# Optimization experiments

Hardware: AMD Instinct MI355X
Metric: run time of the kernel (lower is better)

The kernel has to match this reference:

```python
import jax, jax.numpy as jnp
import numpy as np

B, L = 64, 2048
N_RESTYPE, N_GROUP, N_ATOM = 21, 8, 14


def _compose(R1, t1, R2, t2):
    # rigid compose: (R1,t1) o (R2,t2) = (R1@R2, R1@t2 + t1)
    R = jnp.einsum('...ij,...jk->...ik', R1, R2)
    t = jnp.einsum('...ij,...j->...i', R1, t2) + t1
    return R, t


def setup_inputs() -> dict:
    key = jax.random.key(0)
    ks = jax.random.split(key, 8)
    return {
        'bb_rots': jax.random.normal(ks[0], (B, L, 3, 3), jnp.float32),
        'bb_trans': jax.random.normal(ks[1], (B, L, 3), jnp.float32),
        'angles': jax.random.normal(ks[2], (B, L, 7, 2), jnp.float32),
        'aatype': jax.random.randint(ks[3], (B, L), 0, N_RESTYPE),
        'default_frames': jax.random.normal(ks[4], (N_RESTYPE, N_GROUP, 4, 4), jnp.float32),
        'group_idx': jax.random.randint(ks[5], (N_RESTYPE, N_ATOM), 0, N_GROUP),
        'atom_mask': jax.random.uniform(ks[6], (N_RESTYPE, N_ATOM), jnp.float32),
        'lit_positions': jax.random.normal(ks[7], (N_RESTYPE, N_ATOM, 3), jnp.float32),
    }


def reference(bb_rots, bb_trans, angles, aatype, default_frames, group_idx, atom_mask, lit_positions):
    # ---- torsion_angles_to_frames ----
    d4 = default_frames[aatype]                      # [B,L,8,4,4]
    dR, dt = d4[..., :3, :3], d4[..., :3, 3]
    # prepend identity backbone torsion (sin=0, cos=1)
    bb = jnp.broadcast_to(jnp.array([0.0, 1.0], angles.dtype), (*angles.shape[:-2], 1, 2))
    ang = jnp.concatenate([bb, angles], axis=-2)     # [B,L,8,2]
    s, c = ang[..., 0], ang[..., 1]
    z, o = jnp.zeros_like(s), jnp.ones_like(s)
    # rotation about x-axis built from (sin, cos)
    rotx = jnp.stack([
        jnp.stack([o, z, z], axis=-1),
        jnp.stack([z, c, -s], axis=-1),
        jnp.stack([z, s, c], axis=-1),
    ], axis=-2)                                      # [B,L,8,3,3]
    fR = jnp.einsum('blgij,blgjk->blgik', dR, rotx)  # default_r.compose(all_rots)
    ft = dt                                          # all_rots has zero translation
    # chain chi2..chi4 onto chi1
    R5, t5 = _compose(fR[:, :, 4], ft[:, :, 4], fR[:, :, 5], ft[:, :, 5])
    R6, t6 = _compose(R5, t5, fR[:, :, 6], ft[:, :, 6])
    R7, t7 = _compose(R6, t6, fR[:, :, 7], ft[:, :, 7])
    Rbb = jnp.concatenate([fR[:, :, :5], R5[:, :, None], R6[:, :, None], R7[:, :, None]], axis=2)
    tbb = jnp.concatenate([ft[:, :, :5], t5[:, :, None], t6[:, :, None], t7[:, :, None]], axis=2)
    # compose with global backbone frame
    Rg = jnp.einsum('blij,blgjk->blgik', bb_rots, Rbb)          # [B,L,8,3,3]
    tg = jnp.einsum('blij,blgj->blgi', bb_rots, tbb) + bb_trans[:, :, None]

    # ---- frames_and_literature_positions_to_atom14_pos ----
    gidx = group_idx[aatype]                                    # [B,L,14]
    Ra = jnp.take_along_axis(Rg, gidx[:, :, :, None, None], axis=2)  # [B,L,14,3,3]
    ta = jnp.take_along_axis(tg, gidx[:, :, :, None], axis=2)        # [B,L,14,3]
    lit = lit_positions[aatype]                                 # [B,L,14,3]
    mask = atom_mask[aatype][..., None]                         # [B,L,14,1]
    pred = jnp.einsum('blaij,blaj->blai', Ra, lit) + ta
    return pred * mask
```

## Files before the change

kernel.cpp:

```cpp
#include <hip/hip_runtime.h>


constexpr int NRES_TOTAL = 64 * 2048;
constexpr int NRT = 21;
constexpr int NG  = 8;
constexpr int NA  = 14;
constexpr int OUT_F = NA * 3;
constexpr int BLK = 256;
constexpr int OUT_F4 = BLK * OUT_F / 4;

__global__ __launch_bounds__(256) void protein_mapper_kernel(
    const float* __restrict__ bb_rots,
    const float* __restrict__ bb_trans,
    const float* __restrict__ angles,
    const int*   __restrict__ aatype,
    const float* __restrict__ default_frames,
    const int*   __restrict__ group_idx,
    const float* __restrict__ atom_mask,
    const float* __restrict__ lit_positions,
    float* __restrict__ out)
{
    __shared__ float s_frames[128 * NRT];
    __shared__ int   s_gidx[NA * NRT];
    __shared__ float s_mask[NA * NRT];
    __shared__ float s_lit[NA * 3 * NRT];
    __shared__ float s_out[BLK * OUT_F];

    for (int n = threadIdx.x; n < NRT * 128; n += BLK) {
        const int aa = n / 128, j = n % 128;
        s_frames[j * NRT + aa] = default_frames[n];
    }
    for (int n = threadIdx.x; n < NRT * NA; n += BLK) {
        const int aa = n / NA, a = n % NA;
        s_gidx[a * NRT + aa] = group_idx[n];
        s_mask[a * NRT + aa] = atom_mask[n];
    }
    for (int n = threadIdx.x; n < NRT * NA * 3; n += BLK) {
        const int aa = n / (NA * 3), k = n % (NA * 3);
        s_lit[k * NRT + aa] = lit_positions[n];
    }
    __syncthreads();

    const int i = blockIdx.x * BLK + threadIdx.x;
    const int aa = aatype[i];

    float sv[NG], cv[NG];
    sv[0] = 0.0f; cv[0] = 1.0f;
    const float2* angp = reinterpret_cast<const float2*>(angles + (size_t)i * 14);
    #pragma unroll
    for (int g = 1; g < NG; ++g) {
        float2 sc = angp[g - 1];
        sv[g] = sc.x;
        cv[g] = sc.y;
    }

    float G[NG][12];
    #pragma unroll
    for (int g = 0; g < NG; ++g) {
        const float cg = cv[g], sg = sv[g];
        #pragma unroll
        for (int r = 0; r < 3; ++r) {
            const float a0 = s_frames[(g * 16 + r * 4 + 0) * NRT + aa];
            const float a1 = s_frames[(g * 16 + r * 4 + 1) * NRT + aa];
            const float a2 = s_frames[(g * 16 + r * 4 + 2) * NRT + aa];
            const float a3 = s_frames[(g * 16 + r * 4 + 3) * NRT + aa];
            G[g][r * 3 + 0] = a0;
            G[g][r * 3 + 1] = cg * a1 + sg * a2;
            G[g][r * 3 + 2] = cg * a2 - sg * a1;
            G[g][9 + r]     = a3;
        }
    }

    #pragma unroll
    for (int g = 5; g < NG; ++g) {
        float Q[12];
        #pragma unroll
        for (int r = 0; r < 3; ++r) {
            const float p0 = G[g - 1][r * 3 + 0];
            const float p1 = G[g - 1][r * 3 + 1];
            const float p2 = G[g - 1][r * 3 + 2];
            #pragma unroll
            for (int cdx = 0; cdx < 3; ++cdx)
                Q[r * 3 + cdx] = p0 * G[g][cdx] + p1 * G[g][3 + cdx] + p2 * G[g][6 + cdx];
            Q[9 + r] = p0 * G[g][9] + p1 * G[g][10] + p2 * G[g][11] + G[g - 1][9 + r];
        }
        #pragma unroll
        for (int k = 0; k < 12; ++k) G[g][k] = Q[k];
    }

    const float* br = bb_rots + (size_t)i * 9;
    const float b00 = br[0], b01 = br[1], b02 = br[2];
    const float b10 = br[3], b11 = br[4], b12 = br[5];
    const float b20 = br[6], b21 = br[7], b22 = br[8];
    const float* btp = bb_trans + (size_t)i * 3;
    const float bt0 = btp[0], bt1 = btp[1], bt2 = btp[2];

    float* my = s_out + threadIdx.x * OUT_F;
    #pragma unroll
    for (int a = 0; a < NA; ++a) {
        const int   ga = s_gidx[a * NRT + aa];
        const float m_ = s_mask[a * NRT + aa];
        const float lx = s_lit[(a * 3 + 0) * NRT + aa];
        const float ly = s_lit[(a * 3 + 1) * NRT + aa];
        const float lz = s_lit[(a * 3 + 2) * NRT + aa];
        const bool b0_ = ga & 1, b1_ = ga & 2, b2_ = ga & 4;
        float S[12];
        #pragma unroll
        for (int e = 0; e < 12; ++e) {
            const float t0 = b0_ ? G[1][e] : G[0][e];
            const float t1 = b0_ ? G[3][e] : G[2][e];
            const float t2 = b0_ ? G[5][e] : G[4][e];
            const float t3 = b0_ ? G[7][e] : G[6][e];
            const float u0 = b1_ ? t1 : t0;
            const float u1 = b1_ ? t3 : t2;
            S[e] = b2_ ? u1 : u0;
        }
        const float px = S[0] * lx + S[1] * ly + S[2] * lz + S[9];
        const float py = S[3] * lx + S[4] * ly + S[5] * lz + S[10];
        const float pz = S[6] * lx + S[7] * ly + S[8] * lz + S[11];
        my[a * 3 + 0] = (b00 * px + b01 * py + b02 * pz + bt0) * m_;
        my[a * 3 + 1] = (b10 * px + b11 * py + b12 * pz + bt1) * m_;
        my[a * 3 + 2] = (b20 * px + b21 * py + b22 * pz + bt2) * m_;
    }
    __syncthreads();

    const float4* s4 = reinterpret_cast<const float4*>(s_out);
    float4* o4 = reinterpret_cast<float4*>(out + (size_t)blockIdx.x * (BLK * OUT_F));
    for (int j = threadIdx.x; j < OUT_F4; j += BLK)
        o4[j] = s4[j];
}

extern "C" void kernel_launch(void* const* d_in, const int* in_sizes, int n_in,
                              void* d_out, int out_size, void* d_ws, size_t ws_size,
                              hipStream_t stream) {
    const float* bb_rots        = (const float*)d_in[0];
    const float* bb_trans       = (const float*)d_in[1];
    const float* angles         = (const float*)d_in[2];
    const int*   aatype         = (const int*)d_in[3];
    const float* default_frames = (const float*)d_in[4];
    const int*   group_idx      = (const int*)d_in[5];
    const float* atom_mask      = (const float*)d_in[6];
    const float* lit_positions  = (const float*)d_in[7];
    float* out = (float*)d_out;

    const int blocks = NRES_TOTAL / BLK;
    protein_mapper_kernel<<<blocks, BLK, 0, stream>>>(
        bb_rots, bb_trans, angles, aatype,
        default_frames, group_idx, atom_mask, lit_positions, out);
}
```

Baseline: 93.90 us.

## Split each residue across four threads and write output directly

Each residue is now handled by four threads, each computing up to four atoms, so the grid grows fourfold. The shared-memory output staging buffer and its second barrier are removed in favour of direct float2 stores. Per-residue global loads are issued before the shared-table fill to overlap latency. The cost is that the frame construction and chi composition are computed redundantly four times per residue, and the shared tables are loaded by four times as many blocks.

```diff
diff --git a/kernel.cpp b/kernel.cpp
--- a/kernel.cpp
+++ b/kernel.cpp
@@ -5,9 +5,8 @@
 constexpr int NRT = 21;
 constexpr int NG  = 8;
 constexpr int NA  = 14;
-constexpr int OUT_F = NA * 3;
 constexpr int BLK = 256;
-constexpr int OUT_F4 = BLK * OUT_F / 4;
+constexpr int RPB = BLK / 4;
 
 __global__ __launch_bounds__(256) void protein_mapper_kernel(
     const float* __restrict__ bb_rots,
@@ -24,35 +23,46 @@
     __shared__ int   s_gidx[NA * NRT];
     __shared__ float s_mask[NA * NRT];
     __shared__ float s_lit[NA * 3 * NRT];
-    __shared__ float s_out[BLK * OUT_F];
 
-    for (int n = threadIdx.x; n < NRT * 128; n += BLK) {
+    const int t   = threadIdx.x;
+    const int res = blockIdx.x * RPB + (t >> 2);
+    const int sub = t & 3;
+
+    const int aa_early = aatype[res];
+    float2 ang[7];
+    {
+        const float2* angp = reinterpret_cast<const float2*>(angles + (size_t)res * 14);
+        #pragma unroll
+        for (int g = 0; g < 7; ++g) ang[g] = angp[g];
+    }
+    const float* br = bb_rots + (size_t)res * 9;
+    const float b00 = br[0], b01 = br[1], b02 = br[2];
+    const float b10 = br[3], b11 = br[4], b12 = br[5];
+    const float b20 = br[6], b21 = br[7], b22 = br[8];
+    const float* btp = bb_trans + (size_t)res * 3;
+    const float bt0 = btp[0], bt1 = btp[1], bt2 = btp[2];
+
+    for (int n = t; n < NRT * 128; n += BLK) {
         const int aa = n / 128, j = n % 128;
         s_frames[j * NRT + aa] = default_frames[n];
     }
-    for (int n = threadIdx.x; n < NRT * NA; n += BLK) {
+    for (int n = t; n < NRT * NA; n += BLK) {
         const int aa = n / NA, a = n % NA;
         s_gidx[a * NRT + aa] = group_idx[n];
         s_mask[a * NRT + aa] = atom_mask[n];
     }
-    for (int n = threadIdx.x; n < NRT * NA * 3; n += BLK) {
+    for (int n = t; n < NRT * NA * 3; n += BLK) {
         const int aa = n / (NA * 3), k = n % (NA * 3);
         s_lit[k * NRT + aa] = lit_positions[n];
     }
     __syncthreads();
 
-    const int i = blockIdx.x * BLK + threadIdx.x;
-    const int aa = aatype[i];
+    const int aa = aa_early;
 
     float sv[NG], cv[NG];
     sv[0] = 0.0f; cv[0] = 1.0f;
-    const float2* angp = reinterpret_cast<const float2*>(angles + (size_t)i * 14);
     #pragma unroll
-    for (int g = 1; g < NG; ++g) {
-        float2 sc = angp[g - 1];
-        sv[g] = sc.x;
-        cv[g] = sc.y;
-    }
+    for (int g = 1; g < NG; ++g) { sv[g] = ang[g - 1].x; cv[g] = ang[g - 1].y; }
 
     float G[NG][12];
     #pragma unroll
@@ -88,46 +98,46 @@
         for (int k = 0; k < 12; ++k) G[g][k] = Q[k];
     }
 
-    const float* br = bb_rots + (size_t)i * 9;
-    const float b00 = br[0], b01 = br[1], b02 = br[2];
-    const float b10 = br[3], b11 = br[4], b12 = br[5];
-    const float b20 = br[6], b21 = br[7], b22 = br[8];
-    const float* btp = bb_trans + (size_t)i * 3;
-    const float bt0 = btp[0], bt1 = btp[1], bt2 = btp[2];
+    float q[12];
+    #pragma unroll
+    for (int j = 0; j < 4; ++j) {
+        const int a = 4 * sub + j;
+        if (a < NA) {
+            const int   ga = s_gidx[a * NRT + aa];
+            const float m_ = s_mask[a * NRT + aa];
+            const float lx = s_lit[(a * 3 + 0) * NRT + aa];
+            const float ly = s_lit[(a * 3 + 1) * NRT + aa];
+            const float lz = s_lit[(a * 3 + 2) * NRT + aa];
+            const bool b0_ = ga & 1, b1_ = ga & 2, b2_ = ga & 4;
+            float S[12];
+            #pragma unroll
+            for (int e = 0; e < 12; ++e) {
+                const float t0 = b0_ ? G[1][e] : G[0][e];
+                const float t1 = b0_ ? G[3][e] : G[2][e];
+                const float t2 = b0_ ? G[5][e] : G[4][e];
+                const float t3 = b0_ ? G[7][e] : G[6][e];
+                const float u0 = b1_ ? t1 : t0;
+                const float u1 = b1_ ? t3 : t2;
+                S[e] = b2_ ? u1 : u0;
+            }
+            const float px = S[0] * lx + S[1] * ly + S[2] * lz + S[9];
+            const float py = S[3] * lx + S[4] * ly + S[5] * lz + S[10];
+            const float pz = S[6] * lx + S[7] * ly + S[8] * lz + S[11];
+            q[j * 3 + 0] = (b00 * px + b01 * py + b02 * pz + bt0) * m_;
+            q[j * 3 + 1] = (b10 * px + b11 * py + b12 * pz + bt1) * m_;
+            q[j * 3 + 2] = (b20 * px + b21 * py + b22 * pz + bt2) * m_;
+        }
+    }
 
-    float* my = s_out + threadIdx.x * OUT_F;
+    float2* o2 = reinterpret_cast<float2*>(out) + (size_t)res * 21 + sub * 6;
+    const int nf2 = (sub == 3) ? 3 : 6;
     #pragma unroll
-    for (int a = 0; a < NA; ++a) {
-        const int   ga = s_gidx[a * NRT + aa];
-        const float m_ = s_mask[a * NRT + aa];
-        const float lx = s_lit[(a * 3 + 0) * NRT + aa];
-        const float ly = s_lit[(a * 3 + 1) * NRT + aa];
-        const float lz = s_lit[(a * 3 + 2) * NRT + aa];
-        const bool b0_ = ga & 1, b1_ = ga & 2, b2_ = ga & 4;
-        float S[12];
-        #pragma unroll
-        for (int e = 0; e < 12; ++e) {
-            const float t0 = b0_ ? G[1][e] : G[0][e];
-            const float t1 = b0_ ? G[3][e] : G[2][e];
-            const float t2 = b0_ ? G[5][e] : G[4][e];
-            const float t3 = b0_ ? G[7][e] : G[6][e];
-            const float u0 = b1_ ? t1 : t0;
-            const float u1 = b1_ ? t3 : t2;
-            S[e] = b2_ ? u1 : u0;
+    for (int k = 0; k < 6; ++k) {
+        if (k < nf2) {
+            float2 v; v.x = q[2 * k + 0]; v.y = q[2 * k + 1];
+            o2[k] = v;
         }
-        const float px = S[0] * lx + S[1] * ly + S[2] * lz + S[9];
-        const float py = S[3] * lx + S[4] * ly + S[5] * lz + S[10];
-        const float pz = S[6] * lx + S[7] * ly + S[8] * lz + S[11];
-        my[a * 3 + 0] = (b00 * px + b01 * py + b02 * pz + bt0) * m_;
-        my[a * 3 + 1] = (b10 * px + b11 * py + b12 * pz + bt1) * m_;
-        my[a * 3 + 2] = (b20 * px + b21 * py + b22 * pz + bt2) * m_;
     }
-    __syncthreads();
-
-    const float4* s4 = reinterpret_cast<const float4*>(s_out);
-    float4* o4 = reinterpret_cast<float4*>(out + (size_t)blockIdx.x * (BLK * OUT_F));
-    for (int j = threadIdx.x; j < OUT_F4; j += BLK)
-        o4[j] = s4[j];
 }
 
 extern "C" void kernel_launch(void* const* d_in, const int* in_sizes, int n_in,
@@ -143,7 +153,7 @@
     const float* lit_positions  = (const float*)d_in[7];
     float* out = (float*)d_out;
 
-    const int blocks = NRES_TOTAL / BLK;
+    const int blocks = NRES_TOTAL / RPB;
     protein_mapper_kernel<<<blocks, BLK, 0, stream>>>(
         bb_rots, bb_trans, angles, aatype,
         default_frames, group_idx, atom_mask, lit_positions, out);
```

Result: slower. 106.5 us (+13.4%).
